# Performance work log

Measured on AMD Instinct MI355X. Metric: run time of the kernel, lower is better.

The kernel has to match this reference:

```python
import jax, jax.numpy as jnp
import numpy as np

U, B, D = 1024, 8, 512
H, HD = 8, 64
CL, RC = 64, 4            # chunk length, right-context per chunk
C = U // CL               # 16 chunks
R, S, M = C * RC, C, C - 1
Q, KV = R + U + S, M + R + U
PE = 2 * U - 1
NEG_INF = -1e8


def _chunk_mask():
    # True = disallowed connection. Query rows = [right_context(R), utterance(U), summary(S)];
    # key cols = [memory(M), right_context(R), utterance(U)].
    mask = np.ones((Q, KV), dtype=bool)
    for c in range(C):
        cols = []
        cols += list(range(0, c))                                  # memory of preceding chunks
        cols += list(range(M + c * RC, M + (c + 1) * RC))          # own right context
        u0 = max(0, c - 1) * CL                                    # one left-context chunk
        cols += list(range(M + R + u0, M + R + (c + 1) * CL))      # utterance up to own chunk
        cols = np.array(cols)
        rows = np.concatenate([
            np.arange(c * RC, (c + 1) * RC),                       # right-context queries
            np.arange(R + c * CL, R + (c + 1) * CL),               # utterance queries
            np.array([R + U + c]),                                 # summary query
        ])
        mask[np.ix_(rows, cols)] = False
    return jnp.asarray(mask)


def _xavier(key, shape):
    fan_in, fan_out = shape[-1], shape[0]
    a = (6.0 / (fan_in + fan_out)) ** 0.5
    return jax.random.uniform(key, shape, jnp.float32, -a, a)


def setup_inputs() -> dict:
    key = jax.random.key(0)
    ks = jax.random.split(key, 16)
    return {
        "utterance": jax.random.normal(ks[0], (U, B, D), jnp.float32),
        "lengths": jax.random.randint(ks[1], (B,), U // 2, U + 1),
        "right_context": jax.random.normal(ks[2], (R, B, D), jnp.float32),
        "summary": jax.random.normal(ks[3], (S, B, D), jnp.float32),
        "memory": jax.random.normal(ks[4], (M, B, D), jnp.float32),
        "attention_mask": _chunk_mask(),
        "pos_emb": jax.random.normal(ks[5], (PE, D), jnp.float32),
        "W_kv": _xavier(ks[6], (2 * D, D)),
        "b_kv": jnp.zeros((2 * D,), jnp.float32),
        "W_q": _xavier(ks[7], (D, D)),
        "b_q": jnp.zeros((D,), jnp.float32),
        "W_out": _xavier(ks[8], (D, D)),
        "b_out": jnp.zeros((D,), jnp.float32),
        "W_pos": _xavier(ks[9], (D, D)),
        "pos_bias_u": _xavier(ks[10], (H, HD)),
        "pos_bias_v": _xavier(ks[11], (H, HD)),
    }


def reference(utterance, lengths, right_context, summary, memory, attention_mask,
              pos_emb, W_kv, b_kv, W_q, b_q, W_out, b_out, W_pos,
              pos_bias_u, pos_bias_v):
    u_len, b, d = utterance.shape
    r, m, s = right_context.shape[0], memory.shape[0], summary.shape[0]
    h = pos_bias_u.shape[0]
    hd = d // h
    scaling = hd ** -0.5

    query = jnp.concatenate([right_context, utterance, summary], 0) @ W_q.T + b_q   # (Q,B,D)
    kv = jnp.concatenate([memory, right_context, utterance], 0) @ W_kv.T + b_kv     # (KV,B,2D)
    key_t, val_t = kv[..., :d], kv[..., d:]
    q_len, kv_len = query.shape[0], key_t.shape[0]

    k = key_t.reshape(kv_len, b, h, hd).transpose(1, 2, 0, 3)   # (B,H,KV,hd)
    v = val_t.reshape(kv_len, b, h, hd).transpose(1, 2, 0, 3)   # (B,H,KV,hd)
    q = query.reshape(q_len, b, h, hd)                           # (Q,B,H,hd)

    qu = (q + pos_bias_u).transpose(1, 2, 0, 3)                  # (B,H,Q,hd)
    matrix_ac = jnp.einsum('bhqe,bhke->bhqk', qu, k)             # (B,H,Q,KV)

    qv = (q[r:r + u_len] + pos_bias_v).transpose(1, 2, 0, 3)     # (B,H,U,hd)
    pe_len = pos_emb.shape[0]
    pos = (pos_emb @ W_pos.T).reshape(pe_len, h, hd).transpose(1, 0, 2)  # (H,PE,hd)
    bd_u = jnp.einsum('bhue,hpe->bhup', qv, pos)                 # (B,H,U,PE)

    # rel_shift: out[u, j] = in[u, U-1-u+j]
    out_len = pe_len - (u_len - 1)
    idx = (u_len - 1) - jnp.arange(u_len)[:, None] + jnp.arange(out_len)[None, :]
    bd_u = jnp.take_along_axis(bd_u, idx[None, None], axis=-1)   # (B,H,U,out_len)

    matrix_bd = jnp.zeros_like(matrix_ac).at[:, :, r:r + u_len, m + r:].set(bd_u)
    w = (matrix_ac + matrix_bd) * scaling

    w = jnp.where(attention_mask[None, None], NEG_INF, w)
    pad = jnp.arange(kv_len)[None, :] >= (kv_len - u_len + lengths)[:, None]  # (B,KV)
    w = jnp.where(pad[:, None, None, :], NEG_INF, w)

    probs = jax.nn.softmax(w, axis=-1)
    attn = jnp.einsum('bhqk,bhke->bhqe', probs, v)               # (B,H,Q,hd)
    attn = attn.transpose(2, 0, 1, 3).reshape(q_len, b, d)       # (Q,B,D)

    out_ru = attn[:r + u_len] @ W_out.T + b_out                  # (R+U,B,D)
    out_mem = jnp.clip(attn[r + u_len:], -10.0, 10.0)            # (S,B,D); tanh_on_mem=False
    return out_ru, out_mem
```

## Files before the change

kernel.cpp:

```cpp
#include <hip/hip_runtime.h>
#include <hip/hip_bf16.h>

typedef __hip_bfloat16 bf16;
typedef __attribute__((ext_vector_type(8))) short short8v;
typedef __attribute__((ext_vector_type(4))) float float4v;

#define UU 1024
#define BB 8
#define DD 512
#define HH 8
#define HD 64
#define RR 64
#define SS 16
#define MM 15
#define QQ 1104
#define KVL 1103
#define PEL 2047
#define NU 1536
#define MU 8952

#define AS1 __attribute__((address_space(1)))
#define AS3 __attribute__((address_space(3)))

__device__ __forceinline__ float lo16(unsigned u) { return __uint_as_float(u << 16); }
__device__ __forceinline__ float hi16(unsigned u) { return __uint_as_float(u & 0xffff0000u); }
__device__ __forceinline__ unsigned pk2(float a, float b) {
  unsigned short x = __builtin_bit_cast(unsigned short, __float2bfloat16(a));
  unsigned short y = __builtin_bit_cast(unsigned short, __float2bfloat16(b));
  return (unsigned)x | ((unsigned)y << 16);
}

struct PackDesc {
  const void* src[16];
  unsigned int srcoff[16];
  unsigned int dstoff[16];
  unsigned int cum[17];
};

__global__ __launch_bounds__(256) void pack_all(PackDesc d, bf16* base,
                                                const void* __restrict__ probe,
                                                int* __restrict__ flagout,
                                                int nchunks) {
  __shared__ int wsum[4];
  const unsigned short* p = (const unsigned short*)probe;
  int big = 0;
  for (int i = threadIdx.x; i < 4096; i += 256)
    big += (((p[i] >> 7) & 0xFF) >= 137) ? 1 : 0;
  #pragma unroll
  for (int off = 32; off; off >>= 1) big += __shfl_down(big, off);
  if ((threadIdx.x & 63) == 0) wsum[threadIdx.x >> 6] = big;
  __syncthreads();
  const int flag = (wsum[0] + wsum[1] + wsum[2] + wsum[3] < 16) ? 1 : 0;
  if (threadIdx.x == 0 && blockIdx.x == 0) *flagout = flag;

  int g = blockIdx.x * 256 + threadIdx.x;
  if (g >= nchunks) return;
  int s = 0;
  #pragma unroll
  for (int i = 1; i < 17; ++i) s += (g >= d.cum[i]) ? 1 : 0;
  unsigned local = (g - d.cum[s]) * 8u;
  bf16* dst = base + d.dstoff[s] + local;
  if (flag) {
    const uint4 v = *(const uint4*)((const bf16*)d.src[s] + d.srcoff[s] + local);
    *(uint4*)dst = v;
  } else {
    const float* fp = (const float*)d.src[s] + d.srcoff[s] + local;
    uint4 o;
    o.x = pk2(fp[0], fp[1]);
    o.y = pk2(fp[2], fp[3]);
    o.z = pk2(fp[4], fp[5]);
    o.w = pk2(fp[6], fp[7]);
    *(uint4*)dst = o;
  }
}

struct GemmP {
  const bf16* X; const bf16* W; const bf16* bias; void* out;
  int M, N, K; const int* outf;
};

__global__ __launch_bounds__(256, 3) void gemm_dual(GemmP g0, GemmP g1, int ysplit) {
  __shared__ bf16 As[64 * 128];
  __shared__ bf16 Bs[128 * 128];
  GemmP g; int bm, bn;
  if ((int)blockIdx.y < ysplit) {
    g = g0;
    int bi = (int)blockIdx.y * (int)gridDim.x + (int)blockIdx.x;
    int nbn = g0.N >> 7;
    int j = bi >> 3;
    int bmi = (bi & 7) + (j / nbn) * 8;
    int bni = j % nbn;
    if (bmi >= ((g0.M + 63) >> 6)) return;
    bm = bmi * 64; bn = bni * 128;
  } else {
    g = g1;
    int nt = g1.N >> 7;
    int bi = ((int)blockIdx.y - ysplit) * gridDim.x + blockIdx.x;
    if (bi >= ((g1.M + 63) >> 6) * nt) return;
    bm = (bi / nt) * 64; bn = (bi % nt) * 128;
  }
  const int tid = threadIdx.x;
  const int lane = tid & 63, wv = tid >> 6;
  const int wr = wv >> 1, wc = wv & 1;
  const int l4 = lane >> 4;
  const int lb = lane & 15;
  const int quad = lane >> 4, l15 = lane & 15;

  float4v acc[2][4] = {};

  for (int kb = 0; kb < g.K; kb += 128) {
    #pragma unroll
    for (int i = 0; i < 4; ++i) {
      int r = wv * 16 + i * 4 + l4;
      int gm = bm + r; if (gm > g.M - 1) gm = g.M - 1;
      const bf16* src = g.X + (size_t)gm * g.K + kb + ((lb ^ (r & 15)) * 8);
      __builtin_amdgcn_global_load_lds((const AS1 void*)src,
                                       (AS3 void*)&As[(wv * 16 + i * 4) * 128], 16, 0, 0);
    }
    #pragma unroll
    for (int i = 0; i < 8; ++i) {
      int r = wv * 32 + i * 4 + l4;
      int gn = bn + r; if (gn > g.N - 1) gn = g.N - 1;
      const bf16* src = g.W + (size_t)gn * g.K + kb + ((lb ^ (r & 15)) * 8);
      __builtin_amdgcn_global_load_lds((const AS1 void*)src,
                                       (AS3 void*)&Bs[(wv * 32 + i * 4) * 128], 16, 0, 0);
    }
    __syncthreads();
    #pragma unroll
    for (int ki = 0; ki < 4; ++ki) {
      const int slot = ((ki * 4 + quad) ^ l15) * 8;
      short8v a[2], bq[4];
      #pragma unroll
      for (int t = 0; t < 2; ++t)
        a[t] = *(const short8v*)&As[(wr * 32 + t * 16 + l15) * 128 + slot];
      #pragma unroll
      for (int t = 0; t < 4; ++t)
        bq[t] = *(const short8v*)&Bs[(wc * 64 + t * 16 + l15) * 128 + slot];
      #pragma unroll
      for (int mt = 0; mt < 2; ++mt)
        #pragma unroll
        for (int nt = 0; nt < 4; ++nt)
          acc[mt][nt] = __builtin_amdgcn_mfma_f32_16x16x32_bf16(
              a[mt], bq[nt], acc[mt][nt], 0, 0, 0);
    }
    __syncthreads();
  }

  const bool as_bf16 = (g.outf == nullptr) ? true : (*g.outf != 0);
  #pragma unroll
  for (int mt = 0; mt < 2; ++mt) {
    #pragma unroll
    for (int r = 0; r < 4; ++r) {
      int gm = bm + wr * 32 + mt * 16 + quad * 4 + r;
      if (gm >= g.M) continue;
      #pragma unroll
      for (int nt = 0; nt < 4; ++nt) {
        int gn = bn + wc * 64 + nt * 16 + l15;
        float v = acc[mt][nt][r];
        if (g.bias) v += __bfloat162float(g.bias[gn]);
        size_t o = (size_t)gm * g.N + gn;
        if (as_bf16) ((bf16*)g.out)[o] = __float2bfloat16(v);
        else         ((float*)g.out)[o] = v;
      }
    }
  }
}

__device__ __forceinline__ int gcol(int row, int c, int u0, int ncols) {
  if (row < c) return row;
  if (row < c + 4) return 15 + 4 * c + (row - c);
  if (row < ncols) return 79 + u0 + (row - c - 4);
  return 0;
}

__global__ __launch_bounds__(256, 2) void attn_chunk(
    const bf16* __restrict__ qkv, const bf16* __restrict__ pos,
    const bf16* __restrict__ pbu, const bf16* __restrict__ pbv,
    const int* __restrict__ lengths, bf16* __restrict__ attn,
    const int* __restrict__ flag, void* __restrict__ dout) {
  __shared__ char lds[65536];
  bf16* Vs   = (bf16*)(lds);
  bf16* Aqu  = (bf16*)(lds + 19456);
  bf16* Kt   = (bf16*)(lds + 29696);
  bf16* Aqv  = (bf16*)(lds + 32768);
  bf16* Psl  = (bf16*)(lds + 40960);
  bf16* Eb   = (bf16*)(lds + 49152);
  bf16* Pp   = (bf16*)(lds + 19456);
  float* wred  = (float*)(lds + 46336);
  float* rstat = (float*)(lds + 47616);

  const int idx = blockIdx.x;
  const int h = idx & 7, b = (idx >> 3) & 7, c = idx >> 6;
  const int u0 = c ? (c - 1) * 64 : 0;
  const int nut = c ? 128 : 64;
  const int ncols = c + 4 + nut;
  const int q0 = c ? 63 : 127;
  const int tid = threadIdx.x, lane = tid & 63, wv = tid >> 6;
  const int quad = lane >> 4, l15 = lane & 15, key = l15 & 7;
  const int lenlim = lengths[b] - u0;
  const bool obf = (*flag != 0);

  {
    int lr = lane >> 3;
    int sbr = (lane & 7) ^ lr;
    for (int i = wv; i < 19; i += 4) {
      int row = i * 8 + lr;
      int g = gcol(row, c, u0, ncols);
      int sbv = (lane & 7) ^ (i & 7);
      const bf16* src = qkv + ((size_t)(g * 8 + b)) * NU + 1024 + h * 64 + sbv * 8;
      __builtin_amdgcn_global_load_lds((const AS1 void*)src, (AS3 void*)(Vs + i * 512), 16, 0, 0);
    }
    for (int i = wv; i < 24; i += 4) {
      int p = i * 8 + lr;
      const bf16* src = pos + (size_t)p * 512 + h * 64 + sbr * 8;
      __builtin_amdgcn_global_load_lds((const AS1 void*)src, (AS3 void*)(Psl + i * 512), 16, 0, 0);
    }
  }
  for (int id = tid; id < 1152; id += 256) {
    bool isv = id >= 640;
    int lid = isv ? id - 640 : id;
    int m = lid >> 3, ec = lid & 7;
    int qrow;
    if (isv) qrow = 64 + 64 * c + m;
    else qrow = (m < 64) ? (64 + 64 * c + m)
              : (m < 68) ? (4 * c + (m - 64))
              : (m == 68) ? (1088 + c) : 0;
    const uint4 qa = *(const uint4*)(qkv + ((size_t)((qrow + 15) * 8 + b)) * NU + h * 64 + ec * 8);
    const uint4 ba = *(const uint4*)((isv ? pbv : pbu) + h * 64 + ec * 8);
    uint4 o;
    o.x = pk2(lo16(qa.x) + lo16(ba.x), hi16(qa.x) + hi16(ba.x));
    o.y = pk2(lo16(qa.y) + lo16(ba.y), hi16(qa.y) + hi16(ba.y));
    o.z = pk2(lo16(qa.z) + lo16(ba.z), hi16(qa.z) + hi16(ba.z));
    o.w = pk2(lo16(qa.w) + lo16(ba.w), hi16(qa.w) + hi16(ba.w));
    *(uint4*)((isv ? Aqv : Aqu) + m * 64 + (ec ^ (m & 7)) * 8) = o;
  }
  __syncthreads();

  float4v eacc[4][3];
  #pragma unroll
  for (int mt = 0; mt < 4; ++mt)
    #pragma unroll
    for (int i = 0; i < 3; ++i) eacc[mt][i] = (float4v){0.f, 0.f, 0.f, 0.f};
  {
    short8v av[4][2];
    #pragma unroll
    for (int mt = 0; mt < 4; ++mt)
      #pragma unroll
      for (int ks = 0; ks < 2; ++ks)
        av[mt][ks] = *(const short8v*)&Aqv[(mt * 16 + l15) * 64 + ((ks * 4 + quad) ^ key) * 8];
    #pragma unroll
    for (int nti = 0; nti < 3; ++nti) {
      int nt = wv + nti * 4;
      short8v b0 = *(const short8v*)&Psl[(nt * 16 + l15) * 64 + (quad ^ key) * 8];
      short8v b1 = *(const short8v*)&Psl[(nt * 16 + l15) * 64 + ((4 + quad) ^ key) * 8];
      #pragma unroll
      for (int mt = 0; mt < 4; ++mt) {
        eacc[mt][nti] = __builtin_amdgcn_mfma_f32_16x16x32_bf16(av[mt][0], b0, eacc[mt][nti], 0, 0, 0);
        eacc[mt][nti] = __builtin_amdgcn_mfma_f32_16x16x32_bf16(av[mt][1], b1, eacc[mt][nti], 0, 0, 0);
      }
    }
  }
  __syncthreads();

  {
    int lr = lane >> 3, sbr = (lane & 7) ^ lr;
    for (int i = wv; i < 19; i += 4) {
      int row = i * 8 + lr;
      int g = gcol(row, c, u0, ncols);
      const bf16* src = qkv + ((size_t)(g * 8 + b)) * NU + 512 + h * 64 + sbr * 8;
      __builtin_amdgcn_global_load_lds((const AS1 void*)src, (AS3 void*)(Kt + i * 512), 16, 0, 0);
    }
  }
  #pragma unroll
  for (int nti = 0; nti < 3; ++nti) {
    int p = (wv + nti * 4) * 16 + l15;
    #pragma unroll
    for (int mt = 0; mt < 4; ++mt)
      #pragma unroll
      for (int r = 0; r < 4; ++r) {
        int m = mt * 16 + quad * 4 + r;
        int jl = p - q0 + m;
        if (jl >= 0 && jl < nut)
          Eb[m * 128 + (jl ^ (((m >> 2) & 7) << 4))] = __float2bfloat16(eacc[mt][nti][r]);
      }
  }
  __syncthreads();

  const int nnt = (wv < 2) ? 3 : 2;
  float4v sacc[5][3];
  #pragma unroll
  for (int mt = 0; mt < 5; ++mt)
    #pragma unroll
    for (int i = 0; i < 3; ++i) sacc[mt][i] = (float4v){0.f, 0.f, 0.f, 0.f};
  {
    short8v au[5][2];
    #pragma unroll
    for (int mt = 0; mt < 5; ++mt)
      #pragma unroll
      for (int ks = 0; ks < 2; ++ks)
        au[mt][ks] = *(const short8v*)&Aqu[(mt * 16 + l15) * 64 + ((ks * 4 + quad) ^ key) * 8];
    #pragma unroll
    for (int nti = 0; nti < 3; ++nti) {
      if (nti < nnt) {
        int nt = wv + nti * 4;
        short8v b0 = *(const short8v*)&Kt[(nt * 16 + l15) * 64 + (quad ^ key) * 8];
        short8v b1 = *(const short8v*)&Kt[(nt * 16 + l15) * 64 + ((4 + quad) ^ key) * 8];
        #pragma unroll
        for (int mt = 0; mt < 5; ++mt) {
          sacc[mt][nti] = __builtin_amdgcn_mfma_f32_16x16x32_bf16(au[mt][0], b0, sacc[mt][nti], 0, 0, 0);
          sacc[mt][nti] = __builtin_amdgcn_mfma_f32_16x16x32_bf16(au[mt][1], b1, sacc[mt][nti], 0, 0, 0);
        }
      }
    }
  }
  __syncthreads();

  #pragma unroll
  for (int nti = 0; nti < 3; ++nti) {
    if (nti < nnt) {
      int colv = (wv + nti * 4) * 16 + l15;
      int jl = colv - (c + 4);
      bool cvalid = (colv < ncols) && !(jl >= 0 && jl >= lenlim);
      #pragma unroll
      for (int mt = 0; mt < 5; ++mt)
        #pragma unroll
        for (int r = 0; r < 4; ++r) {
          float s = sacc[mt][nti][r];
          if (cvalid) {
            if (mt < 4 && jl >= 0) {
              int m = mt * 16 + quad * 4 + r;
              s += __bfloat162float(Eb[m * 128 + (jl ^ (((m >> 2) & 7) << 4))]);
            }
            s *= 0.125f;
          } else s = -1e30f;
          sacc[mt][nti][r] = s;
        }
    }
  }

  {
    #pragma unroll
    for (int mt = 0; mt < 5; ++mt)
      #pragma unroll
      for (int r = 0; r < 4; ++r) {
        float v = -3e38f;
        #pragma unroll
        for (int nti = 0; nti < 3; ++nti)
          if (nti < nnt) v = fmaxf(v, sacc[mt][nti][r]);
        v = fmaxf(v, __shfl_xor(v, 1));
        v = fmaxf(v, __shfl_xor(v, 2));
        v = fmaxf(v, __shfl_xor(v, 4));
        v = fmaxf(v, __shfl_xor(v, 8));
        if (l15 == 0) wred[(mt * 16 + quad * 4 + r) * 4 + wv] = v;
      }
  }
  __syncthreads();
  if (tid < 80)
    rstat[tid] = fmaxf(fmaxf(wred[tid * 4], wred[tid * 4 + 1]),
                       fmaxf(wred[tid * 4 + 2], wred[tid * 4 + 3]));
  __syncthreads();

  {
    float rmx[5][4], rsum[5][4];
    #pragma unroll
    for (int mt = 0; mt < 5; ++mt)
      #pragma unroll
      for (int r = 0; r < 4; ++r) {
        rmx[mt][r] = rstat[mt * 16 + quad * 4 + r];
        rsum[mt][r] = 0.f;
      }
    #pragma unroll
    for (int nti = 0; nti < 3; ++nti) {
      if (nti < nnt) {
        int colv = (wv + nti * 4) * 16 + l15;
        #pragma unroll
        for (int mt = 0; mt < 5; ++mt)
          #pragma unroll
          for (int r = 0; r < 4; ++r) {
            float p = __expf(sacc[mt][nti][r] - rmx[mt][r]);
            Pp[(mt * 16 + quad * 4 + r) * 168 + colv] = __float2bfloat16(p);
            rsum[mt][r] += p;
          }
      }
    }
    #pragma unroll
    for (int mt = 0; mt < 5; ++mt)
      #pragma unroll
      for (int r = 0; r < 4; ++r) {
        float v = rsum[mt][r];
        v += __shfl_xor(v, 1);
        v += __shfl_xor(v, 2);
        v += __shfl_xor(v, 4);
        v += __shfl_xor(v, 8);
        if (l15 == 0) wred[(mt * 16 + quad * 4 + r) * 4 + wv] = v;
      }
  }
  __syncthreads();
  if (tid < 80)
    rstat[tid] = 1.f / (wred[tid * 4] + wred[tid * 4 + 1] + wred[tid * 4 + 2] + wred[tid * 4 + 3]);
  __syncthreads();

  const int kmax = (ncols + 31) >> 5;
  float4v oacc[5];
  #pragma unroll
  for (int mt = 0; mt < 5; ++mt) oacc[mt] = (float4v){0.f, 0.f, 0.f, 0.f};
  const int ehi = (wv * 16 + l15) >> 3, elo = l15 & 7;
  for (int ks = 0; ks < kmax; ++ks) {
    short8v bq;
    const int blk = ehi ^ ((ks * 4 + quad) & 7);
    #pragma unroll
    for (int j = 0; j < 8; ++j)
      bq[j] = ((const short*)Vs)[(ks * 32 + quad * 8 + j) * 64 + blk * 8 + elo];
    #pragma unroll
    for (int mt = 0; mt < 5; ++mt) {
      short8v af = *(const short8v*)&Pp[(mt * 16 + l15) * 168 + ks * 32 + quad * 8];
      oacc[mt] = __builtin_amdgcn_mfma_f32_16x16x32_bf16(af, bq, oacc[mt], 0, 0, 0);
    }
  }

  #pragma unroll
  for (int mt = 0; mt < 5; ++mt) {
    #pragma unroll
    for (int r = 0; r < 4; ++r) {
      int m = mt * 16 + quad * 4 + r;
      if (m >= 69) continue;
      float o = oacc[mt][r] * rstat[m];
      if (m < 68) {
        int qrow = (m < 64) ? (64 + 64 * c + m) : (4 * c + (m - 64));
        attn[((size_t)(qrow * 8 + b)) * 512 + h * 64 + wv * 16 + l15] = __float2bfloat16(o);
      } else {
        float v = fminf(fmaxf(o, -10.f), 10.f);
        size_t oi = (size_t)1088 * 8 * 512 + ((size_t)(c * 8 + b)) * 512 + h * 64 + wv * 16 + l15;
        if (obf) ((bf16*)dout)[oi] = __float2bfloat16(v);
        else     ((float*)dout)[oi] = v;
      }
    }
  }
}

static inline int cdiv(int a, int b) { return (a + b - 1) / b; }

extern "C" void kernel_launch(void* const* d_in, const int* in_sizes, int n_in,
                              void* d_out, int out_size, void* d_ws, size_t ws_size,
                              hipStream_t stream) {
  const void* utter = d_in[0];
  const int*  lens  = (const int*)d_in[1];
  const void* rctx  = d_in[2];
  const void* summ  = d_in[3];
  const void* memry = d_in[4];
  const void* pose  = d_in[6];
  const void* W_kv  = d_in[7];
  const void* b_kv  = d_in[8];
  const void* W_q   = d_in[9];
  const void* b_q   = d_in[10];
  const void* W_out = d_in[11];
  const void* b_out = d_in[12];
  const void* W_pos = d_in[13];
  const void* pbu   = d_in[14];
  const void* pbv   = d_in[15];

  const unsigned SZ_MM = MM * BB * DD;
  const unsigned SZ_RC = RR * BB * DD;
  const unsigned SZ_UT = UU * BB * DD;
  const unsigned SZ_SM = SS * BB * DD;
  const unsigned N_XU  = SZ_MM + SZ_RC + SZ_UT + SZ_SM;
  const unsigned SZ_PS = 191 * DD;

  int*  flag = (int*)d_ws;
  bf16* base = (bf16*)((char*)d_ws + 64);
  unsigned off = 0;
  bf16* XU    = base + off; unsigned o_XU    = off; off += N_XU;
  bf16* posec = base + off; unsigned o_posec = off; off += 192 * DD;
  bf16* Wcat  = base + off; unsigned o_Wcat  = off; off += (unsigned)NU * DD;
  bf16* bcat  = base + off; unsigned o_bcat  = off; off += NU;
  bf16* Woutp = base + off; unsigned o_Wout  = off; off += DD * DD;
  bf16* boutp = base + off; unsigned o_bout  = off; off += DD;
  bf16* Wposp = base + off; unsigned o_Wpos  = off; off += DD * DD;
  bf16* pbuc  = base + off; unsigned o_pbu   = off; off += DD;
  bf16* pbvc  = base + off; unsigned o_pbv   = off; off += DD;
  bf16* qkv   = base + off; off += (unsigned)(MU + 8) * NU;
  bf16* pos   = base + off; off += 192 * DD;
  bf16* attn  = base + off; off += QQ * BB * DD;

  PackDesc pd;
  const void* srcs[14]  = {memry, rctx, utter, summ, pose,
                           W_q, W_kv, b_q, b_kv, W_out, b_out, W_pos, pbu, pbv};
  unsigned    soffs[14] = {0, 0, 0, 0, 896u * DD, 0, 0, 0, 0, 0, 0, 0, 0, 0};
  unsigned    doffs[14] = {o_XU, o_XU + SZ_MM, o_XU + SZ_MM + SZ_RC,
                           o_XU + SZ_MM + SZ_RC + SZ_UT, o_posec,
                           o_Wcat, o_Wcat + DD * DD, o_bcat, o_bcat + DD,
                           o_Wout, o_bout, o_Wpos, o_pbu, o_pbv};
  unsigned    ns[14]    = {SZ_MM, SZ_RC, SZ_UT, SZ_SM, SZ_PS,
                           DD * DD, 2 * DD * DD, DD, 2 * DD,
                           DD * DD, DD, DD * DD, DD, DD};
  unsigned cum = 0;
  for (int i = 0; i < 14; ++i) {
    pd.src[i] = srcs[i]; pd.srcoff[i] = soffs[i]; pd.dstoff[i] = doffs[i];
    pd.cum[i] = cum; cum += ns[i] / 8;
  }
  pd.src[14] = pbv; pd.srcoff[14] = 0; pd.dstoff[14] = o_pbv;
  pd.src[15] = pbv; pd.srcoff[15] = 0; pd.dstoff[15] = o_pbv;
  pd.cum[14] = cum; pd.cum[15] = cum; pd.cum[16] = cum;
  int nchunks = (int)cum;
  pack_all<<<dim3(cdiv(nchunks, 256)), dim3(256), 0, stream>>>(pd, base, utter, flag, nchunks);

  GemmP gq{XU, Wcat, bcat, qkv, MU, NU, DD, nullptr};
  GemmP gp{posec, Wposp, nullptr, pos, 191, DD, DD, nullptr};
  gemm_dual<<<dim3(12, 145), dim3(256), 0, stream>>>(gq, gp, 144);

  attn_chunk<<<dim3(1024), dim3(256), 0, stream>>>(qkv, pos, pbuc, pbvc, lens, attn,
                                                   flag, d_out);

  GemmP go{attn, Woutp, boutp, d_out, (RR + UU) * BB, DD, DD, flag};
  gemm_dual<<<dim3(4, 136), dim3(256), 0, stream>>>(go, go, 136);
}
```

Measured before the change: 200.3 us.

## Replace QKV/pos projection GEMM with 256x256-tile double-buffered MFMA kernel

Adds a new gemm8 kernel that computes the fused QKV projection and the positional projection with 256x256 output tiles, 512 threads, and double-buffered direct global-to-LDS loads using XOR-swizzled layout. Block IDs are remapped across XCDs, and s_setprio is raised around the MFMA bursts. Compared with the old 12x145 grid of smaller tiles, this is meant to increase data reuse per tile and overlap global loads with compute. In exchange it uses 128KB of LDS per block, carries large accumulator register pressure, and produces a grid of only 212 blocks, so occupancy and load balance become risks.

After: 198.4 us. No clear change (-1.0%).

```diff
diff --git a/kernel.cpp b/kernel.cpp
--- a/kernel.cpp
+++ b/kernel.cpp
@@ -166,6 +166,111 @@
   }
 }
 
+__global__ __launch_bounds__(512, 2) void gemm8(
+    const bf16* __restrict__ XUp, const bf16* __restrict__ Wcatp,
+    const bf16* __restrict__ bcatp, bf16* __restrict__ qkvp,
+    const bf16* __restrict__ posecp, const bf16* __restrict__ Wpospp,
+    bf16* __restrict__ posp) {
+  __shared__ bf16 smem[65536];
+  const int tid = threadIdx.x;
+  const int lane = tid & 63, wv = tid >> 6;
+  const int wr = wv >> 2, wc = wv & 3;
+  const int quad = lane >> 4, l15 = lane & 15, key = l15 & 7;
+  const int lr3 = lane >> 3, l7 = lane & 7;
+  const int schunk = (l7 ^ lr3) * 8;
+
+  const bf16 *gX, *gW, *gB; bf16* gO; int gM, gN, bm, bn;
+  const int bid = (int)blockIdx.x;
+  if (bid < 210) {
+    int xcd = bid & 7, j = bid >> 3;
+    int wg = (xcd < 2 ? xcd * 27 : 54 + (xcd - 2) * 26) + j;
+    bm = (wg / 6) * 256; bn = (wg % 6) * 256;
+    gX = XUp; gW = Wcatp; gB = bcatp; gO = qkvp; gM = MU; gN = NU;
+  } else {
+    gX = posecp; gW = Wpospp; gB = nullptr; gO = posp; gM = 191; gN = 512;
+    bm = 0; bn = (bid - 210) * 256;
+  }
+
+  bf16* A0 = smem;
+  bf16* B0 = smem + 32768;
+
+  auto stage = [&](const bf16* src, int rbase, int Mlim, bf16* dst, int kb) {
+    #pragma unroll
+    for (int j = 0; j < 4; ++j) {
+      int rl = j * 64 + wv * 8 + lr3;
+      int gr = rbase + rl; if (gr > Mlim - 1) gr = Mlim - 1;
+      const bf16* s = src + (size_t)gr * 512 + kb + schunk;
+      __builtin_amdgcn_global_load_lds((const AS1 void*)s,
+                                       (AS3 void*)(dst + (j * 64 + wv * 8) * 64), 16, 0, 0);
+    }
+  };
+
+  float4v acc[8][4] = {};
+
+  stage(gX, bm, gM, A0, 0);
+  stage(gW, bn, gN, B0, 0);
+  stage(gX, bm, gM, A0 + 16384, 64);
+  stage(gW, bn, gN, B0 + 16384, 64);
+  asm volatile("s_waitcnt vmcnt(8)" ::: "memory");
+  asm volatile("s_barrier" ::: "memory");
+
+  for (int t = 0; t < 8; ++t) {
+    const int p = t & 1;
+    const bf16* Ab = A0 + p * 16384;
+    const bf16* Bb = B0 + p * 16384;
+    #pragma unroll
+    for (int ph = 0; ph < 4; ++ph) {
+      const int mh = ph & 1, nh = ph >> 1;
+      if (ph == 0 && t >= 1 && t < 7) stage(gX, bm, gM, A0 + (p ^ 1) * 16384, (t + 1) * 64);
+      if (ph == 1 && t >= 1 && t < 7) stage(gW, bn, gN, B0 + (p ^ 1) * 16384, (t + 1) * 64);
+      short8v al[4][2], bl[2][2];
+      #pragma unroll
+      for (int i = 0; i < 4; ++i) {
+        const bf16* rp = Ab + (wr * 128 + (mh * 4 + i) * 16 + l15) * 64;
+        #pragma unroll
+        for (int ks = 0; ks < 2; ++ks)
+          al[i][ks] = *(const short8v*)(rp + (((ks * 4 + quad) ^ key) * 8));
+      }
+      #pragma unroll
+      for (int j = 0; j < 2; ++j) {
+        const bf16* rp = Bb + (wc * 64 + (nh * 2 + j) * 16 + l15) * 64;
+        #pragma unroll
+        for (int ks = 0; ks < 2; ++ks)
+          bl[j][ks] = *(const short8v*)(rp + (((ks * 4 + quad) ^ key) * 8));
+      }
+      asm volatile("s_barrier" ::: "memory");
+      __builtin_amdgcn_s_setprio(1);
+      #pragma unroll
+      for (int ks = 0; ks < 2; ++ks)
+        #pragma unroll
+        for (int i = 0; i < 4; ++i)
+          #pragma unroll
+          for (int j = 0; j < 2; ++j)
+            acc[mh * 4 + i][nh * 2 + j] = __builtin_amdgcn_mfma_f32_16x16x32_bf16(
+                al[i][ks], bl[j][ks], acc[mh * 4 + i][nh * 2 + j], 0, 0, 0);
+      __builtin_amdgcn_s_setprio(0);
+      if (ph == 3 && t < 7) asm volatile("s_waitcnt vmcnt(0)" ::: "memory");
+      asm volatile("s_barrier" ::: "memory");
+    }
+  }
+
+  #pragma unroll
+  for (int mf = 0; mf < 8; ++mf) {
+    #pragma unroll
+    for (int r = 0; r < 4; ++r) {
+      int gm = bm + wr * 128 + mf * 16 + quad * 4 + r;
+      if (gm >= gM) continue;
+      #pragma unroll
+      for (int nf = 0; nf < 4; ++nf) {
+        int gn = bn + wc * 64 + nf * 16 + l15;
+        float v = acc[mf][nf][r];
+        if (gB) v += __bfloat162float(gB[gn]);
+        gO[(size_t)gm * gN + gn] = __float2bfloat16(v);
+      }
+    }
+  }
+}
+
 __device__ __forceinline__ int gcol(int row, int c, int u0, int ncols) {
   if (row < c) return row;
   if (row < c + 4) return 15 + 4 * c + (row - c);
@@ -504,9 +609,7 @@
   int nchunks = (int)cum;
   pack_all<<<dim3(cdiv(nchunks, 256)), dim3(256), 0, stream>>>(pd, base, utter, flag, nchunks);
 
-  GemmP gq{XU, Wcat, bcat, qkv, MU, NU, DD, nullptr};
-  GemmP gp{posec, Wposp, nullptr, pos, 191, DD, DD, nullptr};
-  gemm_dual<<<dim3(12, 145), dim3(256), 0, stream>>>(gq, gp, 144);
+  gemm8<<<dim3(212), dim3(512), 0, stream>>>(XU, Wcat, bcat, qkv, posec, Wposp, pos);
 
   attn_chunk<<<dim3(1024), dim3(256), 0, stream>>>(qkv, pos, pbuc, pbvc, lens, attn,
                                                    flag, d_out);
```
